# Optimization experiments

Measured on AMD Instinct MI355X. Metric: run time of the kernel, lower is better.

The kernel has to match this reference:

```python
import jax, jax.numpy as jnp
import numpy as np

B, S, L, T = 32, 512, 20, 16
E, H, D = 300, 128, 128
V = 50000
SEG = S // T


def _gru_dir(x, Wi, Wh, bi, bh, reverse):
    """One direction of torch-style GRU. x: (B,S,E). Returns (outs (B,S,H), h_final (B,H))."""
    xs = jnp.swapaxes(x, 0, 1)  # (S,B,E)
    h0 = jnp.zeros((x.shape[0], H), x.dtype)

    def step(h, x_t):
        gi = x_t @ Wi.T + bi          # (B,3H) gates order: r,z,n (torch)
        gh = h @ Wh.T + bh
        r = jax.nn.sigmoid(gi[:, :H] + gh[:, :H])
        z = jax.nn.sigmoid(gi[:, H:2 * H] + gh[:, H:2 * H])
        n = jnp.tanh(gi[:, 2 * H:] + r * gh[:, 2 * H:])
        h_new = (1.0 - z) * n + z * h
        return h_new, h_new

    hN, hs = jax.lax.scan(step, h0, xs, reverse=reverse)
    return jnp.swapaxes(hs, 0, 1), hN


def setup_inputs() -> dict:
    key = jax.random.key(0)
    ks = jax.random.split(key, 16)
    word_ids = jax.random.randint(ks[0], (B, S, L), 0, V, dtype=jnp.int32)
    # contiguous, full-coverage topic segments, 1-based boundaries (as in the torch code)
    starts = jnp.tile(jnp.arange(T, dtype=jnp.int32) * SEG + 1, (B, 1))
    ends = jnp.tile((jnp.arange(T, dtype=jnp.int32) + 1) * SEG, (B, 1))
    sent2topic = jnp.tile((jnp.arange(S, dtype=jnp.int32) // SEG), (B, 1))
    sc = 0.08
    return {
        "word_ids": word_ids, "starts": starts, "ends": ends, "sent2topic": sent2topic,
        "embed_table": jax.random.normal(ks[1], (V, E), jnp.float32) * 0.6,
        "Wi_f": jax.random.normal(ks[2], (3 * H, E), jnp.float32) * sc,
        "Wh_f": jax.random.normal(ks[3], (3 * H, H), jnp.float32) * sc,
        "bi_f": jax.random.normal(ks[4], (3 * H,), jnp.float32) * sc,
        "bh_f": jax.random.normal(ks[5], (3 * H,), jnp.float32) * sc,
        "Wi_b": jax.random.normal(ks[6], (3 * H, E), jnp.float32) * sc,
        "Wh_b": jax.random.normal(ks[7], (3 * H, H), jnp.float32) * sc,
        "bi_b": jax.random.normal(ks[8], (3 * H,), jnp.float32) * sc,
        "bh_b": jax.random.normal(ks[9], (3 * H,), jnp.float32) * sc,
        "W_att": jax.random.normal(ks[10], (4 * H, 4 * H), jnp.float32) * 0.05,
        "v_att": jax.random.normal(ks[11], (4 * H, 1), jnp.float32) * 0.05,
        "W1": jax.random.normal(ks[12], (D, 4 * H), jnp.float32) * 0.05,
        "b1": jax.random.normal(ks[13], (D,), jnp.float32) * 0.05,
        "W2": jax.random.normal(ks[14], (1, D), jnp.float32) * 0.05,
        "b2": jax.random.normal(ks[15], (1,), jnp.float32) * 0.05,
    }


def reference(word_ids, starts, ends, sent2topic, embed_table,
              Wi_f, Wh_f, bi_f, bh_f, Wi_b, Wh_b, bi_b, bh_b,
              W_att, v_att, W1, b1, W2, b2):
    # --- sent_encoder: mean of word embeddings per sentence ---
    sent = jnp.take(embed_table, word_ids, axis=0).mean(axis=2)  # (B,S,E)
    # --- doc_encoder: bidirectional GRU ---
    out_f, h_f = _gru_dir(sent, Wi_f, Wh_f, bi_f, bh_f, reverse=False)
    out_b, h_b = _gru_dir(sent, Wi_b, Wh_b, bi_b, bh_b, reverse=True)
    sent_rep = jnp.concatenate([out_f, out_b], axis=-1)          # (B,S,2H)
    # faithful to torch: hidden (2,B,H).view(B,2H)
    hidden = jnp.stack([h_f, h_b], axis=0)
    doc_rep = hidden.reshape(B, 2 * H)
    doc_rep = jnp.broadcast_to(doc_rep[None], (S, B, 2 * H)).swapaxes(0, 1)  # (B,S,2H)
    # --- topic_rep: boundary diffs (padded index i == 1-based sentence i) ---
    padded = jnp.pad(sent_rep, ((0, 0), (1, 1), (0, 0)))          # (B,S+2,2H)
    g = lambda idx: jnp.take_along_axis(padded, idx[:, :, None], axis=1)  # (B,T,2H)
    fwd_diff = g(ends)[..., :H] - g(starts - 1)[..., :H]
    bwd_diff = g(starts)[..., H:] - g(ends + 1)[..., H:]
    topic_mat = jnp.concatenate([fwd_diff, bwd_diff], axis=-1)   # (B,T,2H)
    topic_rep = jnp.take_along_axis(topic_mat, sent2topic[:, :, None], axis=1)  # (B,S,2H)
    # --- decoder ---
    cat_ds = jnp.concatenate([doc_rep, sent_rep], axis=-1)       # (B,S,4H)
    cat_ts = jnp.concatenate([topic_rep, sent_rep], axis=-1)
    doc_scores = jnp.tanh(cat_ds @ W_att) @ v_att                # (B,S,1)
    topic_scores = jnp.tanh(cat_ts @ W_att) @ v_att
    sum_scores = doc_scores + topic_scores
    doc_w = doc_scores / sum_scores
    topic_w = topic_scores / sum_scores
    context = doc_w * doc_rep + topic_w * topic_rep
    inp = jnp.concatenate([sent_rep, context], axis=-1)          # (B,S,4H)
    h = jax.nn.relu(inp @ W1.T + b1)                             # dropout=eval identity
    logits = (h @ W2.T + b2).squeeze(-1)                         # (B,S)
    return logits
```

## Files before the change

### kernel.cpp

```cpp
#include <hip/hip_runtime.h>


#define LDS_BARRIER() do {                                   \
    asm volatile("s_waitcnt lgkmcnt(0)" ::: "memory");       \
    __builtin_amdgcn_s_barrier();                            \
    asm volatile("" ::: "memory");                           \
  } while (0)

__global__ __launch_bounds__(128) void k_sent_mean(
    const int* __restrict__ wid, const float* __restrict__ emb,
    float* __restrict__ sent)
{
  const int bs = blockIdx.x;
  const int tid = threadIdx.x;
  const int* w = wid + (size_t)bs * 20;
  float a0 = 0.f, a1 = 0.f, a2 = 0.f;
  for (int l = 0; l < 20; ++l) {
    const float* row = emb + (size_t)w[l] * 300;
    a0 += row[tid];
    a1 += row[tid + 128];
    if (tid < 44) a2 += row[tid + 256];
  }
  const float inv = 1.0f / 20.0f;
  float* o = sent + (size_t)bs * 300;
  o[tid] = a0 * inv;
  o[tid + 128] = a1 * inv;
  if (tid < 44) o[tid + 256] = a2 * inv;
}

template<bool BT, int ACT>
__global__ __launch_bounds__(256) void k_gemm(
    const int M, const int N, const int K,
    const float* __restrict__ A, const int lda,
    const float* __restrict__ Bm, const int ldb,
    float* __restrict__ C, const int ldc,
    const float* __restrict__ bias)
{
  (void)N;
  __shared__ float As[64][68];
  __shared__ float Bs[64][68];
  const int tid = threadIdx.x;
  const int m0 = blockIdx.x * 64;
  const int n0 = blockIdx.y * 64;
  const int tx = tid & 15;
  const int ty = tid >> 4;
  float acc[4][4] = {};

  for (int kc = 0; kc < K; kc += 64) {
    const int kb = (K - kc < 64) ? (K - kc) : 64;
    #pragma unroll
    for (int r = 0; r < 4; ++r) {
      const int m = r * 16 + ty;
      const int k4 = tx * 4;
      float4 v = make_float4(0.f, 0.f, 0.f, 0.f);
      if (m0 + m < M) {
        const float* ap = A + (size_t)(m0 + m) * lda + kc;
        if (k4 + 4 <= kb) {
          v = *(const float4*)(ap + k4);
        } else {
          float t0 = (k4 + 0 < kb) ? ap[k4 + 0] : 0.f;
          float t1 = (k4 + 1 < kb) ? ap[k4 + 1] : 0.f;
          float t2 = (k4 + 2 < kb) ? ap[k4 + 2] : 0.f;
          float t3 = (k4 + 3 < kb) ? ap[k4 + 3] : 0.f;
          v = make_float4(t0, t1, t2, t3);
        }
      }
      *(float4*)&As[m][k4] = v;
    }
    if (BT) {
      #pragma unroll
      for (int r = 0; r < 4; ++r) {
        const int n = r * 16 + ty;
        const int k4 = tx * 4;
        float4 v = make_float4(0.f, 0.f, 0.f, 0.f);
        const float* bp = Bm + (size_t)(n0 + n) * ldb + kc;
        if (k4 + 4 <= kb) {
          v = *(const float4*)(bp + k4);
        } else {
          float t0 = (k4 + 0 < kb) ? bp[k4 + 0] : 0.f;
          float t1 = (k4 + 1 < kb) ? bp[k4 + 1] : 0.f;
          float t2 = (k4 + 2 < kb) ? bp[k4 + 2] : 0.f;
          float t3 = (k4 + 3 < kb) ? bp[k4 + 3] : 0.f;
          v = make_float4(t0, t1, t2, t3);
        }
        Bs[k4 + 0][n] = v.x;
        Bs[k4 + 1][n] = v.y;
        Bs[k4 + 2][n] = v.z;
        Bs[k4 + 3][n] = v.w;
      }
    } else {
      #pragma unroll
      for (int r = 0; r < 4; ++r) {
        const int kk = r * 16 + ty;
        const int n4 = tx * 4;
        float4 v = make_float4(0.f, 0.f, 0.f, 0.f);
        if (kk < kb) v = *(const float4*)(Bm + (size_t)(kc + kk) * ldb + n0 + n4);
        *(float4*)&Bs[kk][n4] = v;
      }
    }
    __syncthreads();
    #pragma unroll 4
    for (int kk = 0; kk < kb; ++kk) {
      const float4 bv = *(const float4*)&Bs[kk][tx * 4];
      #pragma unroll
      for (int i = 0; i < 4; ++i) {
        const float a = As[ty * 4 + i][kk];
        acc[i][0] = fmaf(a, bv.x, acc[i][0]);
        acc[i][1] = fmaf(a, bv.y, acc[i][1]);
        acc[i][2] = fmaf(a, bv.z, acc[i][2]);
        acc[i][3] = fmaf(a, bv.w, acc[i][3]);
      }
    }
    __syncthreads();
  }

  float bv4[4] = {0.f, 0.f, 0.f, 0.f};
  if (bias != nullptr) {
    #pragma unroll
    for (int j = 0; j < 4; ++j) bv4[j] = bias[n0 + tx * 4 + j];
  }
  #pragma unroll
  for (int i = 0; i < 4; ++i) {
    const int m = m0 + ty * 4 + i;
    if (m < M) {
      float4 o;
      o.x = acc[i][0] + bv4[0];
      o.y = acc[i][1] + bv4[1];
      o.z = acc[i][2] + bv4[2];
      o.w = acc[i][3] + bv4[3];
      if (ACT == 1) {
        o.x = fmaxf(o.x, 0.f); o.y = fmaxf(o.y, 0.f);
        o.z = fmaxf(o.z, 0.f); o.w = fmaxf(o.w, 0.f);
      }
      *(float4*)&C[(size_t)m * ldc + n0 + tx * 4] = o;
    }
  }
}

__global__ __launch_bounds__(512, 2) void k_gru(
    const float* __restrict__ gi_f, const float* __restrict__ gi_b,
    const float* __restrict__ Wh_f, const float* __restrict__ Wh_b,
    const float* __restrict__ bh_f, const float* __restrict__ bh_b,
    float* __restrict__ srep, float* __restrict__ hfin)
{
  const int dir = blockIdx.x & 1;
  const int b = blockIdx.x >> 1;
  const float* gi = (dir ? gi_b : gi_f) + (size_t)b * 512 * 384;
  const float* Wh = dir ? Wh_b : Wh_f;
  const float* bh = dir ? bh_b : bh_f;

  const int tid = threadIdx.x;
  const int wv = tid >> 6;
  const int ln = tid & 63;
  const int kq = wv & 3;
  const int rg = wv >> 2;
  const int r0 = rg * 192 + ln;

  __shared__ __align__(16) float hlds[128];
  __shared__ float partl[4 * 384];
  __shared__ __align__(16) float gis[2][32 * 384];

  float4 w0[8], w1[8], w2[8];
  {
    const float* p = Wh + (size_t)r0 * 128 + kq * 32;
    #pragma unroll
    for (int kk = 0; kk < 8; ++kk) w0[kk] = *(const float4*)(p + kk * 4);
    p += 64 * 128;
    #pragma unroll
    for (int kk = 0; kk < 8; ++kk) w1[kk] = *(const float4*)(p + kk * 4);
    p += 64 * 128;
    #pragma unroll
    for (int kk = 0; kk < 8; ++kk) w2[kk] = *(const float4*)(p + kk * 4);
  }
  const float bh0 = (kq == 0) ? bh[r0] : 0.f;
  const float bh1 = (kq == 0) ? bh[r0 + 64] : 0.f;
  const float bh2 = (kq == 0) ? bh[r0 + 128] : 0.f;

  {
    const int lo0 = dir ? 480 : 0;
    const float4* g4 = (const float4*)(gi + (size_t)lo0 * 384);
    float4* l4 = (float4*)gis[0];
    #pragma unroll
    for (int j = 0; j < 6; ++j) l4[j * 512 + tid] = g4[j * 512 + tid];
  }
  float hreg = 0.f;
  if (tid < 128) hlds[tid] = 0.f;
  LDS_BARRIER();

  const float4* h4q = (const float4*)hlds + kq * 8;
  float4 stg[6];

  for (int c = 0; c < 16; ++c) {
    const int buf = c & 1;
    const int lo = dir ? (480 - 32 * c) : (32 * c);
    if (c < 15) {
      const int lon = dir ? (480 - 32 * (c + 1)) : (32 * (c + 1));
      const float4* g4 = (const float4*)(gi + (size_t)lon * 384);
      #pragma unroll
      for (int j = 0; j < 6; ++j) stg[j] = g4[j * 512 + tid];
    }

    for (int i = 0; i < 32; ++i) {
      const int sloc = dir ? (31 - i) : i;
      const int seq = lo + sloc;

      float4 A0 = {0.f, 0.f, 0.f, 0.f};
      float4 A1 = {0.f, 0.f, 0.f, 0.f};
      float4 A2 = {0.f, 0.f, 0.f, 0.f};
      #pragma unroll
      for (int kk = 0; kk < 8; ++kk) {
        const float4 hv = h4q[kk];
        A0.x = fmaf(w0[kk].x, hv.x, A0.x);
        A0.y = fmaf(w0[kk].y, hv.y, A0.y);
        A0.z = fmaf(w0[kk].z, hv.z, A0.z);
        A0.w = fmaf(w0[kk].w, hv.w, A0.w);
        A1.x = fmaf(w1[kk].x, hv.x, A1.x);
        A1.y = fmaf(w1[kk].y, hv.y, A1.y);
        A1.z = fmaf(w1[kk].z, hv.z, A1.z);
        A1.w = fmaf(w1[kk].w, hv.w, A1.w);
        A2.x = fmaf(w2[kk].x, hv.x, A2.x);
        A2.y = fmaf(w2[kk].y, hv.y, A2.y);
        A2.z = fmaf(w2[kk].z, hv.z, A2.z);
        A2.w = fmaf(w2[kk].w, hv.w, A2.w);
      }
      partl[kq * 384 + r0]       = (A0.x + A0.y) + (A0.z + A0.w) + bh0;
      partl[kq * 384 + r0 + 64]  = (A1.x + A1.y) + (A1.z + A1.w) + bh1;
      partl[kq * 384 + r0 + 128] = (A2.x + A2.y) + (A2.z + A2.w) + bh2;
      LDS_BARRIER();

      if (tid < 128) {
        const float* grow = &gis[buf][sloc * 384];
        const float ghr = (partl[tid]       + partl[384 + tid])
                        + (partl[768 + tid] + partl[1152 + tid]);
        const float ghz = (partl[tid + 128]        + partl[384 + tid + 128])
                        + (partl[768 + tid + 128]  + partl[1152 + tid + 128]);
        const float ghn = (partl[tid + 256]        + partl[384 + tid + 256])
                        + (partl[768 + tid + 256]  + partl[1152 + tid + 256]);
        const float gir = grow[tid];
        const float giz = grow[tid + 128];
        const float gin = grow[tid + 256];
        const float r = __fdividef(1.f, 1.f + __expf(-(gir + ghr)));
        const float z = __fdividef(1.f, 1.f + __expf(-(giz + ghz)));
        float an = gin + r * ghn;
        an = fminf(fmaxf(an, -15.f), 15.f);
        const float t = __expf(2.f * an);
        const float n = __fdividef(t - 1.f, t + 1.f);
        hreg = (1.f - z) * n + z * hreg;
        hlds[tid] = hreg;
        srep[((size_t)(b * 512 + seq)) * 256 + dir * 128 + tid] = hreg;
      }
      LDS_BARRIER();
    }

    if (c < 15) {
      float4* l4 = (float4*)gis[buf ^ 1];
      #pragma unroll
      for (int j = 0; j < 6; ++j) l4[j * 512 + tid] = stg[j];
      LDS_BARRIER();
    }
  }
  if (tid < 128) hfin[(size_t)dir * 4096 + (size_t)b * 128 + tid] = hreg;
}

__global__ __launch_bounds__(256) void k_topic(
    const int* __restrict__ starts, const int* __restrict__ ends,
    const float* __restrict__ srep, float* __restrict__ tmat)
{
  const int bt = blockIdx.x;
  const int b = bt >> 4;
  const int st = starts[bt], en = ends[bt];
  const int j = threadIdx.x;
  float v;
  if (j < 128) {
    const float a = (en >= 1 && en <= 512) ? srep[((size_t)(b * 512 + en - 1)) * 256 + j] : 0.f;
    const float c = (st - 1 >= 1 && st - 1 <= 512) ? srep[((size_t)(b * 512 + st - 2)) * 256 + j] : 0.f;
    v = a - c;
  } else {
    const float a = (st >= 1 && st <= 512) ? srep[((size_t)(b * 512 + st - 1)) * 256 + j] : 0.f;
    const float c = (en + 1 >= 1 && en + 1 <= 512) ? srep[((size_t)(b * 512 + en)) * 256 + j] : 0.f;
    v = a - c;
  }
  tmat[(size_t)bt * 256 + j] = v;
}

__global__ __launch_bounds__(256) void k_scores(
    const float* spart, const float* __restrict__ docp, const float* __restrict__ topp,
    const float* __restrict__ v_att, const float* __restrict__ srep,
    const float* __restrict__ docrep, const float* __restrict__ tmat,
    const int* __restrict__ s2t, float* inp)
{
  const int bs = blockIdx.x;
  const int b = bs >> 9;
  const int tid = threadIdx.x;
  const int tp = s2t[bs];
  const float* sp = spart + (size_t)bs * 512;
  const float* dp = docp + (size_t)b * 512;
  const float* tq = topp + ((size_t)(b * 16 + tp)) * 512;
  float ds = 0.f, ts = 0.f;
  #pragma unroll
  for (int r = 0; r < 2; ++r) {
    const int o = tid + r * 256;
    const float s0 = sp[o], v = v_att[o];
    ds += tanhf(s0 + dp[o]) * v;
    ts += tanhf(s0 + tq[o]) * v;
  }
  #pragma unroll
  for (int off = 32; off; off >>= 1) {
    ds += __shfl_down(ds, off);
    ts += __shfl_down(ts, off);
  }
  __shared__ float rds[4], rts[4], wsh[2];
  const int wv = tid >> 6, ln = tid & 63;
  if (ln == 0) { rds[wv] = ds; rts[wv] = ts; }
  __syncthreads();
  if (tid == 0) {
    const float D = rds[0] + rds[1] + rds[2] + rds[3];
    const float T = rts[0] + rts[1] + rts[2] + rts[3];
    const float sum = D + T;
    wsh[0] = D / sum;
    wsh[1] = T / sum;
  }
  __syncthreads();
  const float dw = wsh[0], tw = wsh[1];
  const float sr = srep[(size_t)bs * 256 + tid];
  const float ctx = dw * docrep[(size_t)b * 256 + tid]
                  + tw * tmat[((size_t)(b * 16 + tp)) * 256 + tid];
  float* op = inp + (size_t)bs * 512;
  op[tid] = sr;
  op[256 + tid] = ctx;
}

__global__ __launch_bounds__(64) void k_logits(
    const float* __restrict__ hbuf, const float* __restrict__ W2,
    const float* __restrict__ b2, float* __restrict__ out)
{
  const int bs = blockIdx.x;
  const int ln = threadIdx.x;
  const float* h = hbuf + (size_t)bs * 128;
  float a = fmaf(h[ln], W2[ln], h[ln + 64] * W2[ln + 64]);
  #pragma unroll
  for (int off = 32; off; off >>= 1) a += __shfl_down(a, off);
  if (ln == 0) out[bs] = a + b2[0];
}

extern "C" void kernel_launch(void* const* d_in, const int* in_sizes, int n_in,
                              void* d_out, int out_size, void* d_ws, size_t ws_size,
                              hipStream_t stream)
{
  (void)in_sizes; (void)n_in; (void)out_size;

  const int*   word_ids = (const int*)d_in[0];
  const int*   starts   = (const int*)d_in[1];
  const int*   ends     = (const int*)d_in[2];
  const int*   s2t      = (const int*)d_in[3];
  const float* emb      = (const float*)d_in[4];
  const float* Wi_f     = (const float*)d_in[5];
  const float* Wh_f     = (const float*)d_in[6];
  const float* bi_f     = (const float*)d_in[7];
  const float* bh_f     = (const float*)d_in[8];
  const float* Wi_b     = (const float*)d_in[9];
  const float* Wh_b     = (const float*)d_in[10];
  const float* bi_b     = (const float*)d_in[11];
  const float* bh_b     = (const float*)d_in[12];
  const float* W_att    = (const float*)d_in[13];
  const float* v_att    = (const float*)d_in[14];
  const float* W1       = (const float*)d_in[15];
  const float* b1       = (const float*)d_in[16];
  const float* W2       = (const float*)d_in[17];
  const float* b2       = (const float*)d_in[18];
  float* out = (float*)d_out;

  char* ws = (char*)d_ws;
  if (ws_size < 88440832u) return;
  float* sent  = (float*)(ws + 0);
  float* gi_f  = (float*)(ws + 19660800);
  float* gi_b  = (float*)(ws + 44826624);
  float* srep  = (float*)(ws + 69992448);
  float* hfin  = (float*)(ws + 86769664);
  float* tmat  = (float*)(ws + 86802432);
  float* docp  = (float*)(ws + 87326720);
  float* topp  = (float*)(ws + 87392256);
  float* spart = (float*)(ws + 19660800);
  float* hbuf  = (float*)(ws + 0);

  k_sent_mean<<<16384, 128, 0, stream>>>(word_ids, emb, sent);
  k_gemm<true, 0><<<dim3(256, 6), 256, 0, stream>>>(16384, 384, 300, sent, 300, Wi_f, 300, gi_f, 384, bi_f);
  k_gemm<true, 0><<<dim3(256, 6), 256, 0, stream>>>(16384, 384, 300, sent, 300, Wi_b, 300, gi_b, 384, bi_b);
  k_gru<<<64, 512, 0, stream>>>(gi_f, gi_b, Wh_f, Wh_b, bh_f, bh_b, srep, hfin);
  k_topic<<<512, 256, 0, stream>>>(starts, ends, srep, tmat);
  k_gemm<false, 0><<<dim3(256, 8), 256, 0, stream>>>(16384, 512, 256, srep, 256, W_att + 256 * 512, 512, spart, 512, nullptr);
  k_gemm<false, 0><<<dim3(1, 8),   256, 0, stream>>>(32,    512, 256, hfin, 256, W_att,            512, docp,  512, nullptr);
  k_gemm<false, 0><<<dim3(8, 8),   256, 0, stream>>>(512,   512, 256, tmat, 256, W_att,            512, topp,  512, nullptr);
  k_scores<<<16384, 256, 0, stream>>>(spart, docp, topp, v_att, srep, hfin, tmat, s2t, spart);
  k_gemm<true, 1><<<dim3(256, 2), 256, 0, stream>>>(16384, 128, 512, spart, 512, W1, 512, hbuf, 128, b1);
  k_logits<<<16384, 64, 0, stream>>>(hbuf, W2, b2, out);
}
```

Before: 714.2 us.

## Remove second per-step GRU barrier via redundant per-wave gate computation

Each wave now computes the gate nonlinearities and the new hidden state for the 32-element h slice it consumes, and keeps that slice in its own LDS row. This removes the second block-wide barrier per timestep and the barrier after refilling the input-gate staging buffer. The partial-sum LDS buffer is double-buffered by step parity so one barrier per step is enough. Weight registers are pinned with empty asm. In exchange, the gate math runs redundantly across all eight waves, adding transcendental work per step.

```diff
diff --git a/kernel.cpp b/kernel.cpp
--- a/kernel.cpp
+++ b/kernel.cpp
@@ -6,6 +6,10 @@
     __builtin_amdgcn_s_barrier();                            \
     asm volatile("" ::: "memory");                           \
   } while (0)
+
+#define WAIT_LDS() asm volatile("s_waitcnt lgkmcnt(0)" ::: "memory")
+
+#define PIN4(v) asm volatile("" : "+v"(v.x), "+v"(v.y), "+v"(v.z), "+v"(v.w))
 
 __global__ __launch_bounds__(128) void k_sent_mean(
     const int* __restrict__ wid, const float* __restrict__ emb,
@@ -155,9 +159,10 @@
   const int kq = wv & 3;
   const int rg = wv >> 2;
   const int r0 = rg * 192 + ln;
-
-  __shared__ __align__(16) float hlds[128];
-  __shared__ float partl[4 * 384];
+  const int e  = kq * 32 + (ln & 31);
+
+  __shared__ float partl[2][4 * 384];
+  __shared__ __align__(16) float hq[8][32];
   __shared__ __align__(16) float gis[2][32 * 384];
 
   float4 w0[8], w1[8], w2[8];
@@ -172,6 +177,9 @@
     #pragma unroll
     for (int kk = 0; kk < 8; ++kk) w2[kk] = *(const float4*)(p + kk * 4);
   }
+  #pragma unroll
+  for (int kk = 0; kk < 8; ++kk) { PIN4(w0[kk]); PIN4(w1[kk]); PIN4(w2[kk]); }
+
   const float bh0 = (kq == 0) ? bh[r0] : 0.f;
   const float bh1 = (kq == 0) ? bh[r0 + 64] : 0.f;
   const float bh2 = (kq == 0) ? bh[r0 + 128] : 0.f;
@@ -184,10 +192,10 @@
     for (int j = 0; j < 6; ++j) l4[j * 512 + tid] = g4[j * 512 + tid];
   }
   float hreg = 0.f;
-  if (tid < 128) hlds[tid] = 0.f;
-  LDS_BARRIER();
-
-  const float4* h4q = (const float4*)hlds + kq * 8;
+  if (ln < 32) hq[wv][ln] = 0.f;
+  WAIT_LDS();
+
+  const float4* h4 = (const float4*)hq[wv];
   float4 stg[6];
 
   for (int c = 0; c < 16; ++c) {
@@ -201,6 +209,7 @@
     }
 
     for (int i = 0; i < 32; ++i) {
+      const int par = i & 1;
       const int sloc = dir ? (31 - i) : i;
       const int seq = lo + sloc;
 
@@ -209,7 +218,7 @@
       float4 A2 = {0.f, 0.f, 0.f, 0.f};
       #pragma unroll
       for (int kk = 0; kk < 8; ++kk) {
-        const float4 hv = h4q[kk];
+        const float4 hv = h4[kk];
         A0.x = fmaf(w0[kk].x, hv.x, A0.x);
         A0.y = fmaf(w0[kk].y, hv.y, A0.y);
         A0.z = fmaf(w0[kk].z, hv.z, A0.z);
@@ -223,22 +232,24 @@
         A2.z = fmaf(w2[kk].z, hv.z, A2.z);
         A2.w = fmaf(w2[kk].w, hv.w, A2.w);
       }
-      partl[kq * 384 + r0]       = (A0.x + A0.y) + (A0.z + A0.w) + bh0;
-      partl[kq * 384 + r0 + 64]  = (A1.x + A1.y) + (A1.z + A1.w) + bh1;
-      partl[kq * 384 + r0 + 128] = (A2.x + A2.y) + (A2.z + A2.w) + bh2;
+      float* pw = partl[par];
+      pw[kq * 384 + r0]       = (A0.x + A0.y) + (A0.z + A0.w) + bh0;
+      pw[kq * 384 + r0 + 64]  = (A1.x + A1.y) + (A1.z + A1.w) + bh1;
+      pw[kq * 384 + r0 + 128] = (A2.x + A2.y) + (A2.z + A2.w) + bh2;
       LDS_BARRIER();
 
-      if (tid < 128) {
+      {
+        const float* pp = partl[par];
+        const float ghr = (pp[e]       + pp[384 + e])
+                        + (pp[768 + e] + pp[1152 + e]);
+        const float ghz = (pp[e + 128]       + pp[384 + e + 128])
+                        + (pp[768 + e + 128] + pp[1152 + e + 128]);
+        const float ghn = (pp[e + 256]       + pp[384 + e + 256])
+                        + (pp[768 + e + 256] + pp[1152 + e + 256]);
         const float* grow = &gis[buf][sloc * 384];
-        const float ghr = (partl[tid]       + partl[384 + tid])
-                        + (partl[768 + tid] + partl[1152 + tid]);
-        const float ghz = (partl[tid + 128]        + partl[384 + tid + 128])
-                        + (partl[768 + tid + 128]  + partl[1152 + tid + 128]);
-        const float ghn = (partl[tid + 256]        + partl[384 + tid + 256])
-                        + (partl[768 + tid + 256]  + partl[1152 + tid + 256]);
-        const float gir = grow[tid];
-        const float giz = grow[tid + 128];
-        const float gin = grow[tid + 256];
+        const float gir = grow[e];
+        const float giz = grow[e + 128];
+        const float gin = grow[e + 256];
         const float r = __fdividef(1.f, 1.f + __expf(-(gir + ghr)));
         const float z = __fdividef(1.f, 1.f + __expf(-(giz + ghz)));
         float an = gin + r * ghn;
@@ -246,20 +257,23 @@
         const float t = __expf(2.f * an);
         const float n = __fdividef(t - 1.f, t + 1.f);
         hreg = (1.f - z) * n + z * hreg;
-        hlds[tid] = hreg;
-        srep[((size_t)(b * 512 + seq)) * 256 + dir * 128 + tid] = hreg;
-      }
-      LDS_BARRIER();
+        if (ln < 32) {
+          hq[wv][ln] = hreg;
+          if (rg == 0)
+            srep[((size_t)(b * 512 + seq)) * 256 + dir * 128 + e] = hreg;
+        }
+      }
+      WAIT_LDS();
     }
 
     if (c < 15) {
       float4* l4 = (float4*)gis[buf ^ 1];
       #pragma unroll
       for (int j = 0; j < 6; ++j) l4[j * 512 + tid] = stg[j];
-      LDS_BARRIER();
-    }
-  }
-  if (tid < 128) hfin[(size_t)dir * 4096 + (size_t)b * 128 + tid] = hreg;
+    }
+  }
+  if (rg == 0 && ln < 32)
+    hfin[(size_t)dir * 4096 + (size_t)b * 128 + e] = hreg;
 }
 
 __global__ __launch_bounds__(256) void k_topic(
```

Result: slower. 764.3 us (+7.0%).
